# Optimization experiments

Measured on AMD Instinct MI355X. Metric: run time of the kernel, lower is better.

Reference implementation:

```python
import jax, jax.numpy as jnp
import numpy as np

N, D, T = 4096, 256, 8
RHO = 16.0
DT = 1.0 / T


def setup_inputs() -> dict:
    key = jax.random.key(0)
    k1, k2, k3, k4 = jax.random.split(key, 4)
    X = jax.random.normal(k1, (N, D), dtype=jnp.float32)
    # learned deformation parameters (small init so the Euler flow stays stable)
    A = jax.random.normal(k2, (T, N, D), dtype=jnp.float32) * 0.01
    A_aff = jax.random.normal(k3, (T, D, D), dtype=jnp.float32) * 0.01
    b_aff = jax.random.normal(k4, (T, D), dtype=jnp.float32) * 0.01
    return {"X": X, "A": A, "A_aff": A_aff, "b_aff": b_aff}


def _flow(X, A, A_aff, b_aff):
    inv_two_rho2 = 1.0 / (2.0 * RHO * RHO)

    def step(Z, params_t):
        A_t, Aaff_t, baff_t = params_t
        # Gaussian self-kernel K[i,j] = exp(-||z_i - z_j||^2 / (2 rho^2))
        sq = jnp.sum(Z * Z, axis=1)                      # [n]
        dist = sq[:, None] + sq[None, :] - 2.0 * (Z @ Z.T)  # [n, n]
        K = jnp.exp(-dist * inv_two_rho2)
        # velocity: affine part + RKHS (kernel message aggregation) part
        v = Z @ Aaff_t.T + baff_t[None, :] + K @ A_t     # [n, d]
        return Z + DT * v, None

    Z_final, _ = jax.lax.scan(step, X, (A, A_aff, b_aff))
    return Z_final


def reference(X, A, A_aff, b_aff):
    return _flow(X, A, A_aff, b_aff)
```

## Files before the change

kernel.cpp:

```cpp
#include <hip/hip_runtime.h>


#define N_PTS 4096
#define DIM   256
#define DT_C  0.125f
#define C1    (1.0f/512.0f)
#define C2    (1.0f/256.0f)

typedef __bf16 bf16x8 __attribute__((ext_vector_type(8)));
typedef float  f32x16 __attribute__((ext_vector_type(16)));
typedef float  f32x4v __attribute__((ext_vector_type(4)));
typedef unsigned int   u32x4 __attribute__((ext_vector_type(4)));
typedef unsigned short u16x8 __attribute__((ext_vector_type(8)));

__device__ __forceinline__ unsigned short f2bf(float f) {
  unsigned int u = __builtin_bit_cast(unsigned int, f);
  u += 0x7fffu + ((u >> 16) & 1u);
  return (unsigned short)(u >> 16);
}
__device__ __forceinline__ float bf2f(unsigned short s) {
  unsigned int u = ((unsigned int)s) << 16;
  return __builtin_bit_cast(float, u);
}

typedef __attribute__((address_space(1))) const unsigned int gas_u32;
typedef __attribute__((address_space(3))) unsigned int las_u32;
__device__ __forceinline__ void gload_lds16(const void* g, void* l) {
  __builtin_amdgcn_global_load_lds((gas_u32*)g, (las_u32*)l, 16, 0, 0);
}

__global__ __launch_bounds__(256) void k_prep(const float* __restrict__ A,
                                              unsigned short* __restrict__ ATf) {
  __shared__ float sT[64][36];
  const int jgrp = blockIdx.x, ds = blockIdx.y, t = blockIdx.z;
  const int tid = threadIdx.x;
  const float* Ab = A + (size_t)t * N_PTS * DIM;
  {
    const int j_l = tid >> 2, dq = tid & 3;
    const float* src = Ab + (size_t)(jgrp * 64 + j_l) * DIM + ds * 32 + dq * 8;
    f32x4v v0 = *(const f32x4v*)src, v1 = *(const f32x4v*)(src + 4);
    *(f32x4v*)&sT[j_l][dq * 8] = v0;
    *(f32x4v*)&sT[j_l][dq * 8 + 4] = v1;
  }
  __syncthreads();
  const int jb_l = tid >> 6, l = tid & 63, l31 = l & 31, lhi = l >> 5;
  u16x8 o;
#pragma unroll
  for (int e = 0; e < 8; ++e) o[e] = f2bf(sT[jb_l * 16 + lhi * 8 + e][l31]);
  unsigned short* dst = ATf + (size_t)t * (8 * 256 * 64 * 8)
                      + ((size_t)(ds * 256 + jgrp * 4 + jb_l) * 64 + l) * 8;
  *(u16x8*)dst = o;
}

__device__ __forceinline__ int pidx(int r) {
  const int jj = r & 31;
  return (r & ~31) | (((jj >> 2) & 1) << 4) | (((jj >> 3) & 3) << 2) | (jj & 3);
}

__global__ __launch_bounds__(256) void k_init(const float* __restrict__ X,
                                              unsigned short* __restrict__ Zf,
                                              float* __restrict__ erow,
                                              float* __restrict__ eperm) {
  const int tid = threadIdx.x;
  const int r = blockIdx.x * 8 + (tid >> 5), o = tid & 31;
  const size_t base = (size_t)r * DIM + o * 8;
  f32x4v z0 = *(const f32x4v*)(X + base), z1 = *(const f32x4v*)(X + base + 4);
  u16x8 zb; float s = 0.f;
#pragma unroll
  for (int i = 0; i < 4; ++i) { zb[i] = f2bf(z0[i]); zb[4 + i] = f2bf(z1[i]);
                                s += z0[i] * z0[i] + z1[i] * z1[i]; }
  *(u16x8*)(Zf + ((size_t)((r >> 5) * 16 + (o >> 1)) * 64 + (o & 1) * 32 + (r & 31)) * 8) = zb;
#pragma unroll
  for (int d = 16; d > 0; d >>= 1) s += __shfl_down(s, d, 32);
  if (o == 0) { const float e = __expf(-s * C1); erow[r] = e; eperm[pidx(r)] = e; }
}

__global__ __launch_bounds__(256, 2) void k_flash(
    const unsigned short* __restrict__ Zf, const float* __restrict__ erow,
    const float* __restrict__ eperm,
    const unsigned short* __restrict__ ATf_t,
    const float* __restrict__ Aaff_t,
    unsigned short* __restrict__ Opart) {
  __shared__ __align__(16) unsigned short sZj[2][16 * 64 * 8];

  const int tid = threadIdx.x, lane = tid & 63, wid = tid >> 6;
  const int l31 = lane & 31, lhi = lane >> 5;
  const int ig = wid >> 1, dh = wid & 1;
  const int chunk = blockIdx.x;
  const int i0 = blockIdx.y * 64;

  {
    const unsigned short* src = Zf + (size_t)(chunk * 16) * 8192;
#pragma unroll
    for (int p = 0; p < 4; ++p)
      gload_lds16(src + (size_t)(p * 256 + tid) * 8, &sZj[0][(p * 256 + tid) * 8]);
  }

  const unsigned short* zib = Zf + (size_t)(blockIdx.y * 2 + ig) * 8192;
  u32x4 zi[16];
#pragma unroll
  for (int ks = 0; ks < 16; ++ks)
    zi[ks] = *(const u32x4*)(zib + (size_t)ks * 512 + lane * 8);

  const float eI = erow[i0 + ig * 32 + l31];

  f32x16 O[4];
#pragma unroll
  for (int ct = 0; ct < 4; ++ct)
#pragma unroll
    for (int i = 0; i < 16; ++i) O[ct][i] = 0.f;
#pragma unroll
  for (int q = 0; q < 2; ++q) {
    const int ksg = chunk * 2 + q;
    const bf16x8 a = *(const bf16x8*)(zib + (size_t)ksg * 512 + lane * 8);
#pragma unroll
    for (int ct = 0; ct < 4; ++ct) {
      const int d = dh * 128 + ct * 32 + l31;
      const float* bp = Aaff_t + (size_t)d * DIM + ksg * 16 + lhi * 8;
      f32x4v f0 = *(const f32x4v*)bp, f1 = *(const f32x4v*)(bp + 4);
      u16x8 tb;
#pragma unroll
      for (int i = 0; i < 4; ++i) { tb[i] = f2bf(f0[i]); tb[4 + i] = f2bf(f1[i]); }
      O[ct] = __builtin_amdgcn_mfma_f32_32x32x16_bf16(
          a, __builtin_bit_cast(bf16x8, tb), O[ct], 0, 0, 0);
    }
  }
  __syncthreads();

  const float* epc = eperm + (size_t)chunk * 512 + lhi * 16;
  const unsigned short* atb =
      ATf_t + ((size_t)(dh * 4 * 256 + chunk * 32) * 64 + lane) * 8;

  for (int n = 0; n < 16; ++n) {
    const int cur = n & 1;
    if (n < 15) {
      const unsigned short* src = Zf + (size_t)(chunk * 16 + n + 1) * 8192;
#pragma unroll
      for (int p = 0; p < 4; ++p)
        gload_lds16(src + (size_t)(p * 256 + tid) * 8,
                    &sZj[cur ^ 1][(p * 256 + tid) * 8]);
    }
    f32x4v e0 = *(const f32x4v*)(epc + n * 32);
    f32x4v e1 = *(const f32x4v*)(epc + n * 32 + 4);
    f32x4v e2 = *(const f32x4v*)(epc + n * 32 + 8);
    f32x4v e3 = *(const f32x4v*)(epc + n * 32 + 12);
    u32x4 bw0[4];
#pragma unroll
    for (int ct = 0; ct < 4; ++ct)
      bw0[ct] = *(const u32x4*)(atb + ((size_t)ct * 256 + n * 2 + 0) * 512);

    f32x16 Sa, Sb;
#pragma unroll
    for (int i = 0; i < 16; ++i) { Sa[i] = 0.f; Sb[i] = 0.f; }
    __builtin_amdgcn_s_setprio(1);
#pragma unroll
    for (int ks = 0; ks < 16; ks += 2) {
      bf16x8 a0 = *(const bf16x8*)(&sZj[cur][(ks + 0) * 512 + lane * 8]);
      bf16x8 a1 = *(const bf16x8*)(&sZj[cur][(ks + 1) * 512 + lane * 8]);
      Sa = __builtin_amdgcn_mfma_f32_32x32x16_bf16(
          a0, __builtin_bit_cast(bf16x8, zi[ks + 0]), Sa, 0, 0, 0);
      Sb = __builtin_amdgcn_mfma_f32_32x32x16_bf16(
          a1, __builtin_bit_cast(bf16x8, zi[ks + 1]), Sb, 0, 0, 0);
    }
    __builtin_amdgcn_s_setprio(0);

    u32x4 bw1[4];
#pragma unroll
    for (int ct = 0; ct < 4; ++ct)
      bw1[ct] = *(const u32x4*)(atb + ((size_t)ct * 256 + n * 2 + 1) * 512);

    float p[16];
#pragma unroll
    for (int c = 0; c < 16; ++c) {
      const float ej = (c < 4) ? e0[c] : (c < 8) ? e1[c - 4]
                     : (c < 12) ? e2[c - 8] : e3[c - 12];
      p[c] = eI * ej * __expf((Sa[c] + Sb[c]) * C2);
    }
    unsigned int dw[4][2];
#pragma unroll
    for (int g = 0; g < 4; ++g) {
      asm("v_cvt_pk_bf16_f32 %0, %1, %2" : "=v"(dw[g][0]) : "v"(p[4 * g + 0]), "v"(p[4 * g + 1]));
      asm("v_cvt_pk_bf16_f32 %0, %1, %2" : "=v"(dw[g][1]) : "v"(p[4 * g + 2]), "v"(p[4 * g + 3]));
    }
    {
      auto r0 = __builtin_amdgcn_permlane32_swap(dw[0][0], dw[1][0], false, false);
      auto r1 = __builtin_amdgcn_permlane32_swap(dw[0][1], dw[1][1], false, false);
      u32x4 paw; paw[0] = r0[0]; paw[1] = r1[0]; paw[2] = r0[1]; paw[3] = r1[1];
      const bf16x8 pa = __builtin_bit_cast(bf16x8, paw);
      __builtin_amdgcn_s_setprio(1);
#pragma unroll
      for (int ct = 0; ct < 4; ++ct)
        O[ct] = __builtin_amdgcn_mfma_f32_32x32x16_bf16(
            pa, __builtin_bit_cast(bf16x8, bw0[ct]), O[ct], 0, 0, 0);
      __builtin_amdgcn_s_setprio(0);
    }
    {
      auto r0 = __builtin_amdgcn_permlane32_swap(dw[2][0], dw[3][0], false, false);
      auto r1 = __builtin_amdgcn_permlane32_swap(dw[2][1], dw[3][1], false, false);
      u32x4 paw; paw[0] = r0[0]; paw[1] = r1[0]; paw[2] = r0[1]; paw[3] = r1[1];
      const bf16x8 pa = __builtin_bit_cast(bf16x8, paw);
      __builtin_amdgcn_s_setprio(1);
#pragma unroll
      for (int ct = 0; ct < 4; ++ct)
        O[ct] = __builtin_amdgcn_mfma_f32_32x32x16_bf16(
            pa, __builtin_bit_cast(bf16x8, bw1[ct]), O[ct], 0, 0, 0);
      __builtin_amdgcn_s_setprio(0);
    }
    __syncthreads();
  }

  unsigned short* ob = Opart + (size_t)chunk * N_PTS * DIM
                     + (size_t)(i0 + ig * 32) * DIM + dh * 128 + l31;
#pragma unroll
  for (int ct = 0; ct < 4; ++ct)
#pragma unroll
    for (int c = 0; c < 16; ++c) {
      const int row = 4 * lhi + (c & 3) + 8 * (c >> 2);
      ob[(size_t)row * DIM + ct * 32] = f2bf(O[ct][c]);
    }
}

__global__ __launch_bounds__(256) void k_update(const float* __restrict__ Zin,
                                                const unsigned short* __restrict__ Opart,
                                                const float* __restrict__ baff_t,
                                                float* __restrict__ Zout,
                                                unsigned short* __restrict__ Zf,
                                                float* __restrict__ erow,
                                                float* __restrict__ eperm) {
  const int tid = threadIdx.x;
  const int r = blockIdx.x * 8 + (tid >> 5), o = tid & 31;
  const size_t base = (size_t)r * DIM + o * 8;
  f32x4v z0 = *(const f32x4v*)(Zin + base), z1 = *(const f32x4v*)(Zin + base + 4);
  f32x4v s0 = *(const f32x4v*)(baff_t + o * 8), s1 = *(const f32x4v*)(baff_t + o * 8 + 4);
#pragma unroll
  for (int c = 0; c < 8; ++c) {
    u16x8 p = *(const u16x8*)(Opart + (size_t)c * N_PTS * DIM + base);
#pragma unroll
    for (int i = 0; i < 4; ++i) { s0[i] += bf2f(p[i]); s1[i] += bf2f(p[4 + i]); }
  }
  u16x8 zb; float sv = 0.f;
#pragma unroll
  for (int i = 0; i < 4; ++i) {
    z0[i] += DT_C * s0[i]; z1[i] += DT_C * s1[i];
    zb[i] = f2bf(z0[i]); zb[4 + i] = f2bf(z1[i]);
    sv += z0[i] * z0[i] + z1[i] * z1[i];
  }
  *(f32x4v*)(Zout + base) = z0;
  *(f32x4v*)(Zout + base + 4) = z1;
  *(u16x8*)(Zf + ((size_t)((r >> 5) * 16 + (o >> 1)) * 64 + (o & 1) * 32 + (r & 31)) * 8) = zb;
#pragma unroll
  for (int d = 16; d > 0; d >>= 1) sv += __shfl_down(sv, d, 32);
  if (o == 0) { const float e = __expf(-sv * C1); erow[r] = e; eperm[pidx(r)] = e; }
}

extern "C" void kernel_launch(void* const* d_in, const int* in_sizes, int n_in,
                              void* d_out, int out_size, void* d_ws, size_t ws_size,
                              hipStream_t stream) {
  const float* X    = (const float*)d_in[0];
  const float* A    = (const float*)d_in[1];
  const float* Aaff = (const float*)d_in[2];
  const float* baff = (const float*)d_in[3];
  float* out = (float*)d_out;

  char* w = (char*)d_ws;
  size_t off = 0;
  unsigned short* ATf = (unsigned short*)(w + off); off += (size_t)8 * 8 * 256 * 64 * 8 * 2;
  unsigned short* Zf  = (unsigned short*)(w + off); off += (size_t)N_PTS * DIM * 2;
  float* erow  = (float*)(w + off); off += (size_t)N_PTS * 4;
  float* eperm = (float*)(w + off); off += (size_t)N_PTS * 4;
  float* Zf32 = (float*)(w + off); off += (size_t)N_PTS * DIM * 4;
  unsigned short* Opart = (unsigned short*)(w + off); off += (size_t)8 * N_PTS * DIM * 2;
  (void)ws_size; (void)in_sizes; (void)n_in; (void)out_size;

  k_prep<<<dim3(64, 8, 8), 256, 0, stream>>>(A, ATf);
  k_init<<<512, 256, 0, stream>>>(X, Zf, erow, eperm);

  const float* zin = X;
  for (int t = 0; t < 8; ++t) {
    float* zout = (t == 7) ? out : Zf32;
    k_flash<<<dim3(8, 64), 256, 0, stream>>>(
        Zf, erow, eperm, ATf + (size_t)t * (8 * 256 * 64 * 8), Aaff + (size_t)t * DIM * DIM, Opart);
    k_update<<<512, 256, 0, stream>>>(zin, Opart, baff + (size_t)t * DIM, zout, Zf, erow, eperm);
    zin = zout;
  }
}
```

Before: 434.1 us.

## Stream Zj tiles from global into a register ring instead of LDS double buffer

Replaces the LDS double-buffered staging of the Zj key tiles, fed by global_load_lds, with per-wave direct global loads into an 8-deep register ring prefetched ahead of the MFMA consumption. This removes the per-iteration __syncthreads and the LDS reads. In exchange each wave fetches the same tile independently, multiplying L2 traffic, and register pressure rises. The last iteration also prefetches beyond the chunk, which may read past the buffer end.

```diff
diff --git a/kernel.cpp b/kernel.cpp
--- a/kernel.cpp
+++ b/kernel.cpp
@@ -21,12 +21,6 @@
 __device__ __forceinline__ float bf2f(unsigned short s) {
   unsigned int u = ((unsigned int)s) << 16;
   return __builtin_bit_cast(float, u);
-}
-
-typedef __attribute__((address_space(1))) const unsigned int gas_u32;
-typedef __attribute__((address_space(3))) unsigned int las_u32;
-__device__ __forceinline__ void gload_lds16(const void* g, void* l) {
-  __builtin_amdgcn_global_load_lds((gas_u32*)g, (las_u32*)l, 16, 0, 0);
 }
 
 __global__ __launch_bounds__(256) void k_prep(const float* __restrict__ A,
@@ -81,20 +75,18 @@
     const unsigned short* __restrict__ ATf_t,
     const float* __restrict__ Aaff_t,
     unsigned short* __restrict__ Opart) {
-  __shared__ __align__(16) unsigned short sZj[2][16 * 64 * 8];
-
   const int tid = threadIdx.x, lane = tid & 63, wid = tid >> 6;
   const int l31 = lane & 31, lhi = lane >> 5;
   const int ig = wid >> 1, dh = wid & 1;
   const int chunk = blockIdx.x;
   const int i0 = blockIdx.y * 64;
 
-  {
-    const unsigned short* src = Zf + (size_t)(chunk * 16) * 8192;
-#pragma unroll
-    for (int p = 0; p < 4; ++p)
-      gload_lds16(src + (size_t)(p * 256 + tid) * 8, &sZj[0][(p * 256 + tid) * 8]);
-  }
+  const unsigned short* zjs = Zf + (size_t)(chunk * 16) * 8192;
+
+  u32x4 zw[8];
+#pragma unroll
+  for (int f = 0; f < 8; ++f)
+    zw[f] = *(const u32x4*)(zjs + (size_t)f * 512 + lane * 8);
 
   const unsigned short* zib = Zf + (size_t)(blockIdx.y * 2 + ig) * 8192;
   u32x4 zi[16];
@@ -125,21 +117,12 @@
           a, __builtin_bit_cast(bf16x8, tb), O[ct], 0, 0, 0);
     }
   }
-  __syncthreads();
 
   const float* epc = eperm + (size_t)chunk * 512 + lhi * 16;
   const unsigned short* atb =
       ATf_t + ((size_t)(dh * 4 * 256 + chunk * 32) * 64 + lane) * 8;
 
   for (int n = 0; n < 16; ++n) {
-    const int cur = n & 1;
-    if (n < 15) {
-      const unsigned short* src = Zf + (size_t)(chunk * 16 + n + 1) * 8192;
-#pragma unroll
-      for (int p = 0; p < 4; ++p)
-        gload_lds16(src + (size_t)(p * 256 + tid) * 8,
-                    &sZj[cur ^ 1][(p * 256 + tid) * 8]);
-    }
     f32x4v e0 = *(const f32x4v*)(epc + n * 32);
     f32x4v e1 = *(const f32x4v*)(epc + n * 32 + 4);
     f32x4v e2 = *(const f32x4v*)(epc + n * 32 + 8);
@@ -155,12 +138,12 @@
     __builtin_amdgcn_s_setprio(1);
 #pragma unroll
     for (int ks = 0; ks < 16; ks += 2) {
-      bf16x8 a0 = *(const bf16x8*)(&sZj[cur][(ks + 0) * 512 + lane * 8]);
-      bf16x8 a1 = *(const bf16x8*)(&sZj[cur][(ks + 1) * 512 + lane * 8]);
-      Sa = __builtin_amdgcn_mfma_f32_32x32x16_bf16(
-          a0, __builtin_bit_cast(bf16x8, zi[ks + 0]), Sa, 0, 0, 0);
-      Sb = __builtin_amdgcn_mfma_f32_32x32x16_bf16(
-          a1, __builtin_bit_cast(bf16x8, zi[ks + 1]), Sb, 0, 0, 0);
+      const bf16x8 a0 = __builtin_bit_cast(bf16x8, zw[ks & 7]);
+      const bf16x8 a1 = __builtin_bit_cast(bf16x8, zw[(ks + 1) & 7]);
+      Sa = __builtin_amdgcn_mfma_f32_32x32x16_bf16(a0, __builtin_bit_cast(bf16x8, zi[ks + 0]), Sa, 0, 0, 0);
+      Sb = __builtin_amdgcn_mfma_f32_32x32x16_bf16(a1, __builtin_bit_cast(bf16x8, zi[ks + 1]), Sb, 0, 0, 0);
+      zw[ks & 7]       = *(const u32x4*)(zjs + (size_t)(n * 16 + ks + 8) * 512 + lane * 8);
+      zw[(ks + 1) & 7] = *(const u32x4*)(zjs + (size_t)(n * 16 + ks + 9) * 512 + lane * 8);
     }
     __builtin_amdgcn_s_setprio(0);
 
@@ -206,7 +189,6 @@
             pa, __builtin_bit_cast(bf16x8, bw1[ct]), O[ct], 0, 0, 0);
       __builtin_amdgcn_s_setprio(0);
     }
-    __syncthreads();
   }
 
   unsigned short* ob = Opart + (size_t)chunk * N_PTS * DIM
```

After: 788.4 us. 1.82x slower.
